# Kernel optimization log

Hardware: AMD Instinct MI355X
Metric: run time of the kernel (lower is better)

Reference implementation:

```python
import jax, jax.numpy as jnp
import numpy as np

NQ = 4            # num_qubits
DIM = 2 ** NQ     # 16-dim complex state

def _rx(theta):
    c = jnp.cos(theta / 2.0); s = jnp.sin(theta / 2.0)
    return jnp.array([[c, -1j * s], [-1j * s, c]], dtype=jnp.complex64)

def _ry(theta):
    c = jnp.cos(theta / 2.0); s = jnp.sin(theta / 2.0)
    return jnp.array([[c, -s], [s, c]], dtype=jnp.complex64)

def _apply_1q(state, q, U):
    # state: [B, 16] complex; apply 2x2 unitary U on qubit q (qubit 0 = MSB)
    B = state.shape[0]
    st = state.reshape((B,) + (2,) * NQ)
    st = jnp.moveaxis(st, 1 + q, -1)
    st = st @ U.T
    st = jnp.moveaxis(st, -1, 1 + q)
    return st.reshape(B, DIM)

def _apply_cnot(state, c, t):
    # flip target qubit t where control qubit c == 1
    B = state.shape[0]
    st = state.reshape((B,) + (2,) * NQ)
    st = jnp.moveaxis(st, (1 + c, 1 + t), (-2, -1))
    st = jnp.stack([st[..., 0, :], st[..., 1, ::-1]], axis=-2)
    st = jnp.moveaxis(st, (-2, -1), (1 + c, 1 + t))
    return st.reshape(B, DIM)

def _circuit(state):
    rx1, ry1 = _rx(0.1), _ry(0.2)
    rx2, ry2 = _rx(0.3), _ry(0.4)
    for q in range(NQ):
        state = _apply_1q(state, q, rx1)
        state = _apply_1q(state, q, ry1)
    for q in range(NQ - 1):
        state = _apply_cnot(state, q, q + 1)
    for q in range(NQ):
        state = _apply_1q(state, q, rx2)
        state = _apply_1q(state, q, ry2)
    return state

def setup_inputs() -> dict:
    key = jax.random.key(0)
    ks = jax.random.split(key, 9)
    B = 65536
    return {
        'x':   jax.random.normal(ks[0], (B, 784), dtype=jnp.float32),
        'We1': jax.random.normal(ks[1], (784, 256), dtype=jnp.float32) * 0.05,
        'be1': jnp.zeros((256,), dtype=jnp.float32),
        'We2': jax.random.normal(ks[2], (256, 32), dtype=jnp.float32) * 0.05,
        'be2': jnp.zeros((32,), dtype=jnp.float32),
        'W1':  jax.random.normal(ks[3], (32, 128), dtype=jnp.float32) * 0.05,
        'b1':  jnp.zeros((128,), dtype=jnp.float32),
        'W2':  jax.random.normal(ks[4], (128, 10), dtype=jnp.float32) * 0.05,
        'b2':  jnp.zeros((10,), dtype=jnp.float32),
    }

def reference(x, We1, be1, We2, be2, W1, b1, W2, b2):
    # encoder: Linear(784,256) -> ReLU -> Linear(256,32) -> Tanh
    h = jax.nn.relu(x @ We1 + be1)
    enc = jnp.tanh(h @ We2 + be2)               # [B, 32]
    psi = (enc[:, :DIM] + 1j * enc[:, DIM:]).astype(jnp.complex64)
    norm = jnp.sqrt(jnp.sum(jnp.abs(psi) ** 2, axis=1, keepdims=True))
    psi = psi / norm
    psi = _circuit(psi)                          # [B, 16] complex
    feat = jnp.concatenate([psi.real, psi.imag], axis=1)  # [B, 32]
    # classifier: Linear(32,128) -> ReLU -> (Dropout=identity in eval) -> Linear(128,10)
    out = jax.nn.relu(feat @ W1 + b1) @ W2 + b2
    return out
```

## Files before the change

kernel.cpp:

```cpp
#include <hip/hip_runtime.h>
#include <stdint.h>

#define DEVINL __device__ __forceinline__

typedef short bf16x8 __attribute__((ext_vector_type(8)));
typedef float f32x4  __attribute__((ext_vector_type(4)));

DEVINL uint16_t f2bf(float f) {
    uint32_t u = __builtin_bit_cast(uint32_t, f);
    uint32_t r = u + 0x7fffu + ((u >> 16) & 1u);
    return (uint16_t)(r >> 16);
}

DEVINL f32x4 mfma16x16x32(bf16x8 a, bf16x8 b, f32x4 c) {
    return __builtin_amdgcn_mfma_f32_16x16x32_bf16(a, b, c, 0, 0, 0);
}

DEVINL void async_load16(const void* g, void* l) {
    __builtin_amdgcn_global_load_lds(
        (const __attribute__((address_space(1))) void*)g,
        (__attribute__((address_space(3))) void*)l, 16, 0, 0);
}

#define WS_WE1T 0
#define WS_WE2T 409600
#define WS_W1T  425984
#define WS_W2T  434176

__global__ __launch_bounds__(256) void prep_weights(
    const float* __restrict__ We1, const float* __restrict__ We2,
    const float* __restrict__ W1,  const float* __restrict__ W2,
    uint16_t* __restrict__ We1T, uint16_t* __restrict__ We2T,
    uint16_t* __restrict__ W1T,  uint16_t* __restrict__ W2T) {
    int tid = blockIdx.x * 256 + threadIdx.x;
    if (tid < 256 * 800) {
        int n = tid / 800, k = tid % 800;
        We1T[tid] = (k < 784) ? f2bf(We1[k * 256 + n]) : (uint16_t)0;
        return;
    }
    int t2 = tid - 256 * 800;
    if (t2 < 32 * 256) {
        int n = t2 / 256, k = t2 % 256;
        We2T[t2] = f2bf(We2[k * 32 + n]);
        return;
    }
    int t3 = t2 - 32 * 256;
    if (t3 < 128 * 32) {
        int n = t3 / 32, k = t3 % 32;
        W1T[t3] = f2bf(W1[k * 128 + n]);
        return;
    }
    int t4 = t3 - 128 * 32;
    if (t4 < 16 * 128) {
        int n = t4 / 128, k = t4 % 128;
        W2T[t4] = (n < 10) ? f2bf(W2[k * 10 + n]) : (uint16_t)0;
        return;
    }
}

DEVINL void apply_rx(float* sr, float* si, int bit, float c, float s) {
    #pragma unroll
    for (int i = 0; i < 16; i++) {
        if (!(i & bit)) {
            int j = i | bit;
            float r0 = sr[i], i0 = si[i], r1 = sr[j], i1 = si[j];
            sr[i] = c * r0 + s * i1;  si[i] = c * i0 - s * r1;
            sr[j] = c * r1 + s * i0;  si[j] = c * i1 - s * r0;
        }
    }
}
DEVINL void apply_ry(float* sr, float* si, int bit, float c, float s) {
    #pragma unroll
    for (int i = 0; i < 16; i++) {
        if (!(i & bit)) {
            int j = i | bit;
            float r0 = sr[i], i0 = si[i], r1 = sr[j], i1 = si[j];
            sr[i] = c * r0 - s * r1;  si[i] = c * i0 - s * i1;
            sr[j] = s * r0 + c * r1;  si[j] = s * i0 + c * i1;
        }
    }
}
DEVINL void apply_cnot(float* sr, float* si, int cb, int tb) {
    #pragma unroll
    for (int i = 0; i < 16; i++) {
        if ((i & cb) && !(i & tb)) {
            int j = i | tb;
            float tr = sr[i]; sr[i] = sr[j]; sr[j] = tr;
            float ti = si[i]; si[i] = si[j]; si[j] = ti;
        }
    }
}
DEVINL void circuit(float* sr, float* si) {
    const float C1 = 0.99875026039496628f, S1 = 0.04997916927067833f;
    const float C2 = 0.99500416527802582f, S2 = 0.09983341664682815f;
    const float C3 = 0.98877107793604227f, S3 = 0.14943813247359922f;
    const float C4 = 0.98006657784124163f, S4 = 0.19866933079506122f;
    #pragma unroll
    for (int q = 0; q < 4; q++) {
        int bit = 8 >> q;
        apply_rx(sr, si, bit, C1, S1);
        apply_ry(sr, si, bit, C2, S2);
    }
    apply_cnot(sr, si, 8, 4);
    apply_cnot(sr, si, 4, 2);
    apply_cnot(sr, si, 2, 1);
    #pragma unroll
    for (int q = 0; q < 4; q++) {
        int bit = 8 >> q;
        apply_rx(sr, si, bit, C3, S3);
        apply_ry(sr, si, bit, C4, S4);
    }
}

__global__ __launch_bounds__(256, 4) void fused_kernel(
    const float* __restrict__ x, const uint16_t* __restrict__ We1T,
    const float* __restrict__ be1,
    const uint16_t* __restrict__ We2T, const float* __restrict__ be2,
    const uint16_t* __restrict__ W1T, const float* __restrict__ b1,
    const uint16_t* __restrict__ W2T, const float* __restrict__ b2,
    float* __restrict__ out) {
    __shared__ __align__(16) char smem[34816];
    uint16_t* Als   = (uint16_t*)smem;
    uint16_t* Bls   = (uint16_t*)(smem + 4096);
    uint16_t* Htile = (uint16_t*)smem;
    float*    encls  = (float*)smem;
    uint16_t* featls = (uint16_t*)(smem + 8448);
    uint16_t* a1ls   = (uint16_t*)(smem + 13568);

    const int t = threadIdx.x;
    const int rowbase = blockIdx.x * 64;
    const int w  = t >> 6;
    const int l  = t & 63;
    const int lm = l & 15;
    const int lq = l >> 4;

    f32x4 acc[4][4] = {};

    const int ar = t >> 2;
    const int aq = t & 3;
    const float* xrow = x + (size_t)(rowbase + ar) * 784;

    float4 va0 = *(const float4*)(xrow + aq * 8);
    float4 va1 = *(const float4*)(xrow + aq * 8 + 4);

    for (int k0 = 0; k0 < 800; k0 += 32) {
        __syncthreads();

        #pragma unroll
        for (int j = 0; j < 4; j++) {
            int g = j * 256 + t;
            async_load16(We1T + (size_t)(g >> 2) * 800 + (g & 3) * 8 + k0, &Bls[8 * g]);
        }
        union { uint4 u4; uint16_t us[8]; } pk;
        pk.us[0] = f2bf(va0.x); pk.us[1] = f2bf(va0.y);
        pk.us[2] = f2bf(va0.z); pk.us[3] = f2bf(va0.w);
        pk.us[4] = f2bf(va1.x); pk.us[5] = f2bf(va1.y);
        pk.us[6] = f2bf(va1.z); pk.us[7] = f2bf(va1.w);
        *(uint4*)&Als[8 * t] = pk.u4;
        {
            int kn = k0 + 32;
            if (kn < 800) {
                int c = kn + aq * 8;
                if (c < 784) {
                    va0 = *(const float4*)(xrow + c);
                    va1 = *(const float4*)(xrow + c + 4);
                } else {
                    va0 = make_float4(0.f, 0.f, 0.f, 0.f);
                    va1 = make_float4(0.f, 0.f, 0.f, 0.f);
                }
            }
        }
        __syncthreads();

        bf16x8 afr[4], bfr[4];
        #pragma unroll
        for (int mi = 0; mi < 4; mi++)
            afr[mi] = *(const bf16x8*)&Als[(mi * 16 + lm) * 32 + lq * 8];
        #pragma unroll
        for (int ni = 0; ni < 4; ni++)
            bfr[ni] = *(const bf16x8*)&Bls[(w * 64 + ni * 16 + lm) * 32 + lq * 8];
        #pragma unroll
        for (int mi = 0; mi < 4; mi++)
            #pragma unroll
            for (int ni = 0; ni < 4; ni++)
                acc[mi][ni] = mfma16x16x32(afr[mi], bfr[ni], acc[mi][ni]);
    }

    __syncthreads();

    #pragma unroll
    for (int ni = 0; ni < 4; ni++) {
        int n = w * 64 + ni * 16 + lm;
        float bias = be1[n];
        #pragma unroll
        for (int mi = 0; mi < 4; mi++) {
            #pragma unroll
            for (int i = 0; i < 4; i++) {
                int r = mi * 16 + lq * 4 + i;
                float v = acc[mi][ni][i] + bias;
                v = v > 0.f ? v : 0.f;
                Htile[r * 272 + n] = f2bf(v);
            }
        }
    }
    __syncthreads();

    f32x4 acc2[2] = {};
    #pragma unroll
    for (int k0 = 0; k0 < 256; k0 += 32) {
        bf16x8 af = *(const bf16x8*)&Htile[(w * 16 + lm) * 272 + k0 + lq * 8];
        #pragma unroll
        for (int ni = 0; ni < 2; ni++) {
            bf16x8 bf = *(const bf16x8*)&We2T[(ni * 16 + lm) * 256 + k0 + lq * 8];
            acc2[ni] = mfma16x16x32(af, bf, acc2[ni]);
        }
    }
    __syncthreads();

    #pragma unroll
    for (int ni = 0; ni < 2; ni++) {
        int col = ni * 16 + lm;
        float bias = be2[col];
        #pragma unroll
        for (int i = 0; i < 4; i++) {
            int r = w * 16 + lq * 4 + i;
            encls[r * 33 + col] = tanhf(acc2[ni][i] + bias);
        }
    }
    __syncthreads();

    if (t < 64) {
        float e[32];
        #pragma unroll
        for (int j = 0; j < 32; j++) e[j] = encls[t * 33 + j];
        float s = 0.f;
        #pragma unroll
        for (int j = 0; j < 32; j++) s += e[j] * e[j];
        float inv = 1.0f / sqrtf(s);
        float sr[16], si[16];
        #pragma unroll
        for (int i = 0; i < 16; i++) { sr[i] = e[i] * inv; si[i] = e[16 + i] * inv; }
        circuit(sr, si);
        #pragma unroll
        for (int i = 0; i < 16; i++) {
            featls[t * 40 + i]      = f2bf(sr[i]);
            featls[t * 40 + 16 + i] = f2bf(si[i]);
        }
    }
    __syncthreads();

    f32x4 acc3[8] = {};
    {
        bf16x8 af = *(const bf16x8*)&featls[(w * 16 + lm) * 40 + lq * 8];
        #pragma unroll
        for (int ni = 0; ni < 8; ni++) {
            bf16x8 bf = *(const bf16x8*)&W1T[(ni * 16 + lm) * 32 + lq * 8];
            acc3[ni] = mfma16x16x32(af, bf, acc3[ni]);
        }
    }
    #pragma unroll
    for (int ni = 0; ni < 8; ni++) {
        int col = ni * 16 + lm;
        float bias = b1[col];
        #pragma unroll
        for (int i = 0; i < 4; i++) {
            int r = w * 16 + lq * 4 + i;
            float v = acc3[ni][i] + bias;
            v = v > 0.f ? v : 0.f;
            a1ls[r * 136 + col] = f2bf(v);
        }
    }

    f32x4 acc4 = {};
    #pragma unroll
    for (int k0 = 0; k0 < 128; k0 += 32) {
        bf16x8 af = *(const bf16x8*)&a1ls[(w * 16 + lm) * 136 + k0 + lq * 8];
        bf16x8 bf = *(const bf16x8*)&W2T[lm * 128 + k0 + lq * 8];
        acc4 = mfma16x16x32(af, bf, acc4);
    }
    if (lm < 10) {
        float bias = b2[lm];
        #pragma unroll
        for (int i = 0; i < 4; i++) {
            int r = rowbase + w * 16 + lq * 4 + i;
            out[(size_t)r * 10 + lm] = acc4[i] + bias;
        }
    }
}

extern "C" void kernel_launch(void* const* d_in, const int* in_sizes, int n_in,
                              void* d_out, int out_size, void* d_ws, size_t ws_size,
                              hipStream_t stream) {
    const float* x   = (const float*)d_in[0];
    const float* We1 = (const float*)d_in[1];
    const float* be1 = (const float*)d_in[2];
    const float* We2 = (const float*)d_in[3];
    const float* be2 = (const float*)d_in[4];
    const float* W1  = (const float*)d_in[5];
    const float* b1  = (const float*)d_in[6];
    const float* W2  = (const float*)d_in[7];
    const float* b2  = (const float*)d_in[8];
    float* out = (float*)d_out;

    char* ws = (char*)d_ws;
    uint16_t* We1T = (uint16_t*)(ws + WS_WE1T);
    uint16_t* We2T = (uint16_t*)(ws + WS_WE2T);
    uint16_t* W1T  = (uint16_t*)(ws + WS_W1T);
    uint16_t* W2T  = (uint16_t*)(ws + WS_W2T);

    hipLaunchKernelGGL(prep_weights, dim3(856), dim3(256), 0, stream,
                       We1, We2, W1, W2, We1T, We2T, W1T, W2T);
    hipLaunchKernelGGL(fused_kernel, dim3(1024), dim3(256), 0, stream,
                       x, We1T, be1, We2T, be2, W1T, b1, W2T, b2, out);
}
```

Baseline: 323.2 us.

## Double-buffer A tile in LDS and load We1 fragments directly from global

The first GEMM loop now double-buffers the bf16 x tile in LDS, with one barrier per iteration instead of two, and prefetches x two steps ahead. B fragments of We1T are read straight from global memory (L2-resident) into registers instead of being staged through LDS with async loads. This cuts barriers and LDS traffic but exposes global-load latency on the B operand each iteration, and the custom barrier waits only on lgkmcnt, so the global loads are not synchronised by it.

Measured after the change: 337.3 us. 1.04x slower.

```diff
diff --git a/kernel.cpp b/kernel.cpp
--- a/kernel.cpp
+++ b/kernel.cpp
@@ -16,10 +16,8 @@
     return __builtin_amdgcn_mfma_f32_16x16x32_bf16(a, b, c, 0, 0, 0);
 }
 
-DEVINL void async_load16(const void* g, void* l) {
-    __builtin_amdgcn_global_load_lds(
-        (const __attribute__((address_space(1))) void*)g,
-        (__attribute__((address_space(3))) void*)l, 16, 0, 0);
+DEVINL void lds_barrier() {
+    asm volatile("s_waitcnt lgkmcnt(0)\n\ts_barrier" ::: "memory");
 }
 
 #define WS_WE1T 0
@@ -120,8 +118,7 @@
     const uint16_t* __restrict__ W2T, const float* __restrict__ b2,
     float* __restrict__ out) {
     __shared__ __align__(16) char smem[34816];
-    uint16_t* Als   = (uint16_t*)smem;
-    uint16_t* Bls   = (uint16_t*)(smem + 4096);
+    uint16_t* Als = (uint16_t*)smem;
     uint16_t* Htile = (uint16_t*)smem;
     float*    encls  = (float*)smem;
     uint16_t* featls = (uint16_t*)(smem + 8448);
@@ -140,25 +137,43 @@
     const int aq = t & 3;
     const float* xrow = x + (size_t)(rowbase + ar) * 784;
 
-    float4 va0 = *(const float4*)(xrow + aq * 8);
-    float4 va1 = *(const float4*)(xrow + aq * 8 + 4);
-
+    const uint16_t* bbase = We1T + (size_t)(w * 64 + lm) * 800 + lq * 8;
+
+    {
+        float4 v0 = *(const float4*)(xrow + aq * 8);
+        float4 v1 = *(const float4*)(xrow + aq * 8 + 4);
+        union { uint4 u4; uint16_t us[8]; } pk;
+        pk.us[0] = f2bf(v0.x); pk.us[1] = f2bf(v0.y);
+        pk.us[2] = f2bf(v0.z); pk.us[3] = f2bf(v0.w);
+        pk.us[4] = f2bf(v1.x); pk.us[5] = f2bf(v1.y);
+        pk.us[6] = f2bf(v1.z); pk.us[7] = f2bf(v1.w);
+        *(uint4*)&Als[8 * t] = pk.u4;
+    }
+    float4 va0 = *(const float4*)(xrow + 32 + aq * 8);
+    float4 va1 = *(const float4*)(xrow + 32 + aq * 8 + 4);
+    lds_barrier();
+
+    int buf = 0;
     for (int k0 = 0; k0 < 800; k0 += 32) {
-        __syncthreads();
-
-        #pragma unroll
-        for (int j = 0; j < 4; j++) {
-            int g = j * 256 + t;
-            async_load16(We1T + (size_t)(g >> 2) * 800 + (g & 3) * 8 + k0, &Bls[8 * g]);
-        }
-        union { uint4 u4; uint16_t us[8]; } pk;
-        pk.us[0] = f2bf(va0.x); pk.us[1] = f2bf(va0.y);
-        pk.us[2] = f2bf(va0.z); pk.us[3] = f2bf(va0.w);
-        pk.us[4] = f2bf(va1.x); pk.us[5] = f2bf(va1.y);
-        pk.us[6] = f2bf(va1.z); pk.us[7] = f2bf(va1.w);
-        *(uint4*)&Als[8 * t] = pk.u4;
-        {
-            int kn = k0 + 32;
+        const uint16_t* AlsCur = Als + buf * 2048;
+        bf16x8 afr[4];
+        #pragma unroll
+        for (int mi = 0; mi < 4; mi++)
+            afr[mi] = *(const bf16x8*)&AlsCur[(mi * 16 + lm) * 32 + lq * 8];
+
+        bf16x8 bfr[4];
+        #pragma unroll
+        for (int ni = 0; ni < 4; ni++)
+            bfr[ni] = *(const bf16x8*)(bbase + (size_t)(ni * 16) * 800 + k0);
+
+        if (k0 + 32 < 800) {
+            union { uint4 u4; uint16_t us[8]; } pk;
+            pk.us[0] = f2bf(va0.x); pk.us[1] = f2bf(va0.y);
+            pk.us[2] = f2bf(va0.z); pk.us[3] = f2bf(va0.w);
+            pk.us[4] = f2bf(va1.x); pk.us[5] = f2bf(va1.y);
+            pk.us[6] = f2bf(va1.z); pk.us[7] = f2bf(va1.w);
+            *(uint4*)&Als[(buf ^ 1) * 2048 + 8 * t] = pk.u4;
+            int kn = k0 + 64;
             if (kn < 800) {
                 int c = kn + aq * 8;
                 if (c < 784) {
@@ -170,23 +185,16 @@
                 }
             }
         }
-        __syncthreads();
-
-        bf16x8 afr[4], bfr[4];
-        #pragma unroll
-        for (int mi = 0; mi < 4; mi++)
-            afr[mi] = *(const bf16x8*)&Als[(mi * 16 + lm) * 32 + lq * 8];
-        #pragma unroll
-        for (int ni = 0; ni < 4; ni++)
-            bfr[ni] = *(const bf16x8*)&Bls[(w * 64 + ni * 16 + lm) * 32 + lq * 8];
+
         #pragma unroll
         for (int mi = 0; mi < 4; mi++)
             #pragma unroll
             for (int ni = 0; ni < 4; ni++)
                 acc[mi][ni] = mfma16x16x32(afr[mi], bfr[ni], acc[mi][ni]);
-    }
-
-    __syncthreads();
+
+        lds_barrier();
+        buf ^= 1;
+    }
 
     #pragma unroll
     for (int ni = 0; ni < 4; ni++) {
```

## Double-buffer first GEMM LDS tiles with register prefetch and one barrier

Applied to the files above, without the earlier changes.

Replaces the single-buffered first-layer GEMM loop, which used async global-to-LDS loads and two __syncthreads per K step, with double-buffered A/B LDS tiles. The next tile is staged in registers and written into the alternate buffer while the current tile feeds the MFMAs, so each iteration needs only one lightweight lgkmcnt barrier. It also uses nontemporal loads for x, pads the transposed We1 rows to 832, and changes the hidden tile stride to 264. The cost is more LDS and registers, which may reduce occupancy.

Result: slower. 403.6 us (+24.9%).

```diff
diff --git a/kernel.cpp b/kernel.cpp
--- a/kernel.cpp
+++ b/kernel.cpp
@@ -5,6 +5,8 @@
 
 typedef short bf16x8 __attribute__((ext_vector_type(8)));
 typedef float f32x4  __attribute__((ext_vector_type(4)));
+typedef float fvec4  __attribute__((ext_vector_type(4)));
+typedef unsigned int uvec4 __attribute__((ext_vector_type(4)));
 
 DEVINL uint16_t f2bf(float f) {
     uint32_t u = __builtin_bit_cast(uint32_t, f);
@@ -16,16 +18,23 @@
     return __builtin_amdgcn_mfma_f32_16x16x32_bf16(a, b, c, 0, 0, 0);
 }
 
-DEVINL void async_load16(const void* g, void* l) {
-    __builtin_amdgcn_global_load_lds(
-        (const __attribute__((address_space(1))) void*)g,
-        (__attribute__((address_space(3))) void*)l, 16, 0, 0);
+DEVINL bf16x8 pack8(fvec4 v0, fvec4 v1) {
+    union { bf16x8 v; uint16_t us[8]; } pk;
+    pk.us[0] = f2bf(v0[0]); pk.us[1] = f2bf(v0[1]);
+    pk.us[2] = f2bf(v0[2]); pk.us[3] = f2bf(v0[3]);
+    pk.us[4] = f2bf(v1[0]); pk.us[5] = f2bf(v1[1]);
+    pk.us[6] = f2bf(v1[2]); pk.us[7] = f2bf(v1[3]);
+    return pk.v;
+}
+
+DEVINL void lds_barrier() {
+    asm volatile("s_waitcnt lgkmcnt(0)\n\ts_barrier" ::: "memory");
 }
 
 #define WS_WE1T 0
-#define WS_WE2T 409600
-#define WS_W1T  425984
-#define WS_W2T  434176
+#define WS_WE2T 425984
+#define WS_W1T  442368
+#define WS_W2T  450560
 
 __global__ __launch_bounds__(256) void prep_weights(
     const float* __restrict__ We1, const float* __restrict__ We2,
@@ -33,12 +42,12 @@
     uint16_t* __restrict__ We1T, uint16_t* __restrict__ We2T,
     uint16_t* __restrict__ W1T,  uint16_t* __restrict__ W2T) {
     int tid = blockIdx.x * 256 + threadIdx.x;
-    if (tid < 256 * 800) {
-        int n = tid / 800, k = tid % 800;
+    if (tid < 256 * 832) {
+        int n = tid / 832, k = tid % 832;
         We1T[tid] = (k < 784) ? f2bf(We1[k * 256 + n]) : (uint16_t)0;
         return;
     }
-    int t2 = tid - 256 * 800;
+    int t2 = tid - 256 * 832;
     if (t2 < 32 * 256) {
         int n = t2 / 256, k = t2 % 256;
         We2T[t2] = f2bf(We2[k * 32 + n]);
@@ -119,9 +128,9 @@
     const uint16_t* __restrict__ W1T, const float* __restrict__ b1,
     const uint16_t* __restrict__ W2T, const float* __restrict__ b2,
     float* __restrict__ out) {
-    __shared__ __align__(16) char smem[34816];
-    uint16_t* Als   = (uint16_t*)smem;
-    uint16_t* Bls   = (uint16_t*)(smem + 4096);
+    __shared__ __align__(16) char smem[40960];
+    uint16_t* Abuf = (uint16_t*)smem;
+    uint16_t* Bbuf = (uint16_t*)(smem + 8192);
     uint16_t* Htile = (uint16_t*)smem;
     float*    encls  = (float*)smem;
     uint16_t* featls = (uint16_t*)(smem + 8448);
@@ -136,57 +145,78 @@
 
     f32x4 acc[4][4] = {};
 
-    const int ar = t >> 2;
-    const int aq = t & 3;
-    const float* xrow = x + (size_t)(rowbase + ar) * 784;
-
-    float4 va0 = *(const float4*)(xrow + aq * 8);
-    float4 va1 = *(const float4*)(xrow + aq * 8 + 4);
-
-    for (int k0 = 0; k0 < 800; k0 += 32) {
-        __syncthreads();
-
+    const fvec4* xsrc = (const fvec4*)(x + (size_t)(rowbase + (t >> 2)) * 784 + (t & 3) * 8);
+    const int acol = (t & 3) * 8;
+
+    fvec4 aq0, aq1;
+    uvec4 bq[4];
+
+    {
+        fvec4 p0 = __builtin_nontemporal_load(xsrc);
+        fvec4 p1 = __builtin_nontemporal_load(xsrc + 1);
+        *(bf16x8*)&Abuf[t * 8] = pack8(p0, p1);
         #pragma unroll
         for (int j = 0; j < 4; j++) {
-            int g = j * 256 + t;
-            async_load16(We1T + (size_t)(g >> 2) * 800 + (g & 3) * 8 + k0, &Bls[8 * g]);
-        }
-        union { uint4 u4; uint16_t us[8]; } pk;
-        pk.us[0] = f2bf(va0.x); pk.us[1] = f2bf(va0.y);
-        pk.us[2] = f2bf(va0.z); pk.us[3] = f2bf(va0.w);
-        pk.us[4] = f2bf(va1.x); pk.us[5] = f2bf(va1.y);
-        pk.us[6] = f2bf(va1.z); pk.us[7] = f2bf(va1.w);
-        *(uint4*)&Als[8 * t] = pk.u4;
-        {
-            int kn = k0 + 32;
-            if (kn < 800) {
-                int c = kn + aq * 8;
-                if (c < 784) {
-                    va0 = *(const float4*)(xrow + c);
-                    va1 = *(const float4*)(xrow + c + 4);
+            int g = t + 256 * j;
+            bq[j] = *(const uvec4*)(We1T + (size_t)(g >> 2) * 832 + (g & 3) * 8);
+        }
+        #pragma unroll
+        for (int j = 0; j < 4; j++)
+            *(uvec4*)&Bbuf[(t + 256 * j) * 8] = bq[j];
+        aq0 = __builtin_nontemporal_load((const fvec4*)((const float*)xsrc + 32));
+        aq1 = __builtin_nontemporal_load((const fvec4*)((const float*)xsrc + 36));
+        #pragma unroll
+        for (int j = 0; j < 4; j++) {
+            int g = t + 256 * j;
+            bq[j] = *(const uvec4*)(We1T + (size_t)(g >> 2) * 832 + (g & 3) * 8 + 32);
+        }
+    }
+    lds_barrier();
+
+    for (int r = 0; r < 25; ++r) {
+        const uint16_t* As = Abuf + (r & 1) * 2048;
+        const uint16_t* Bs = Bbuf + (r & 1) * 8192;
+
+        bf16x8 afr[4], bfr[4];
+        #pragma unroll
+        for (int mi = 0; mi < 4; mi++)
+            afr[mi] = *(const bf16x8*)&As[(mi * 16 + lm) * 32 + lq * 8];
+        #pragma unroll
+        for (int ni = 0; ni < 4; ni++)
+            bfr[ni] = *(const bf16x8*)&Bs[(w * 64 + ni * 16 + lm) * 32 + lq * 8];
+
+        if (r < 24) {
+            uint16_t* Aw = Abuf + ((r + 1) & 1) * 2048;
+            uint16_t* Bw = Bbuf + ((r + 1) & 1) * 8192;
+            *(bf16x8*)&Aw[t * 8] = pack8(aq0, aq1);
+            #pragma unroll
+            for (int j = 0; j < 4; j++)
+                *(uvec4*)&Bw[(t + 256 * j) * 8] = bq[j];
+            if (r < 23) {
+                int k0 = (r + 2) * 32;
+                int c = k0 + acol;
+                if (c <= 776) {
+                    aq0 = __builtin_nontemporal_load((const fvec4*)((const float*)xsrc + k0));
+                    aq1 = __builtin_nontemporal_load((const fvec4*)((const float*)xsrc + k0 + 4));
                 } else {
-                    va0 = make_float4(0.f, 0.f, 0.f, 0.f);
-                    va1 = make_float4(0.f, 0.f, 0.f, 0.f);
+                    aq0 = (fvec4)(0.f); aq1 = (fvec4)(0.f);
+                }
+                #pragma unroll
+                for (int j = 0; j < 4; j++) {
+                    int g = t + 256 * j;
+                    bq[j] = *(const uvec4*)(We1T + (size_t)(g >> 2) * 832 + (g & 3) * 8 + k0);
                 }
             }
         }
-        __syncthreads();
-
-        bf16x8 afr[4], bfr[4];
-        #pragma unroll
-        for (int mi = 0; mi < 4; mi++)
-            afr[mi] = *(const bf16x8*)&Als[(mi * 16 + lm) * 32 + lq * 8];
-        #pragma unroll
-        for (int ni = 0; ni < 4; ni++)
-            bfr[ni] = *(const bf16x8*)&Bls[(w * 64 + ni * 16 + lm) * 32 + lq * 8];
+
         #pragma unroll
         for (int mi = 0; mi < 4; mi++)
             #pragma unroll
             for (int ni = 0; ni < 4; ni++)
                 acc[mi][ni] = mfma16x16x32(afr[mi], bfr[ni], acc[mi][ni]);
-    }
-
-    __syncthreads();
+
+        lds_barrier();
+    }
 
     #pragma unroll
     for (int ni = 0; ni < 4; ni++) {
@@ -199,7 +229,7 @@
                 int r = mi * 16 + lq * 4 + i;
                 float v = acc[mi][ni][i] + bias;
                 v = v > 0.f ? v : 0.f;
-                Htile[r * 272 + n] = f2bf(v);
+                Htile[r * 264 + n] = f2bf(v);
             }
         }
     }
@@ -208,7 +238,7 @@
     f32x4 acc2[2] = {};
     #pragma unroll
     for (int k0 = 0; k0 < 256; k0 += 32) {
-        bf16x8 af = *(const bf16x8*)&Htile[(w * 16 + lm) * 272 + k0 + lq * 8];
+        bf16x8 af = *(const bf16x8*)&Htile[(w * 16 + lm) * 264 + k0 + lq * 8];
         #pragma unroll
         for (int ni = 0; ni < 2; ni++) {
             bf16x8 bf = *(const bf16x8*)&We2T[(ni * 16 + lm) * 256 + k0 + lq * 8];
@@ -308,7 +338,7 @@
     uint16_t* W1T  = (uint16_t*)(ws + WS_W1T);
     uint16_t* W2T  = (uint16_t*)(ws + WS_W2T);
 
-    hipLaunchKernelGGL(prep_weights, dim3(856), dim3(256), 0, stream,
+    hipLaunchKernelGGL(prep_weights, dim3(888), dim3(256), 0, stream,
                        We1, We2, W1, W2, We1T, We2T, W1T, W2T);
     hipLaunchKernelGGL(fused_kernel, dim3(1024), dim3(256), 0, stream,
                        x, We1T, be1, We2T, be2, W1T, b1, W2T, b2, out);
```
